# Performance work log

Hardware: AMD Instinct MI355X
Metric: run time of the kernel (lower is better)

The kernel has to match this reference:

```python
import jax, jax.numpy as jnp
import numpy as np

B, L, D_MODEL, H, H_DIM = 2, 4096, 768, 1, 128
D_K = H * H_DIM
F_LEN = L // 2 + 1
TEMP = 1.0
EPS = 1e-9
INV_SQRT_DK = float(1.0 / np.sqrt(H_DIM))


def _selector(xc, W1, b1, W2, b2, noise, temp):
    # xc: [B, h, d, F] complex. torch view_as_real(x.transpose(-1,-2))[..., 0] == real part.
    xr = jnp.real(jnp.swapaxes(xc, -1, -2))          # [B, h, F, d]
    h1 = jax.nn.relu(xr @ W1.T + b1)                 # [B, h, F, d//2]
    logit = h1 @ W2.T + b2                           # [B, h, F, 2]
    g = -jnp.log(-jnp.log(noise + EPS) + EPS)        # gumbel noise from uniform input
    z = jax.nn.softmax((logit + g) / temp, axis=-1)[..., 1]  # training mode: soft mask
    return z[..., None, :]                           # [B, h, 1, F]


def _forward(query, key, mask, Wq, bq, Wk, bk, qW1, qb1, qW2, qb2, kW1, kb1, kW2, kb2, q_noise, k_noise):
    nb, Lq = query.shape[0], query.shape[1]
    q = (query @ Wq.T + bq).reshape(nb, Lq, H, H_DIM).transpose(0, 2, 3, 1)  # [B, h, d, L]
    k = (key @ Wk.T + bk).reshape(nb, Lq, H, H_DIM).transpose(0, 2, 3, 1)
    q_tff = jnp.fft.rfft(q, axis=-1)                 # [B, h, d, F] complex
    k_tff = jnp.fft.rfft(k, axis=-1)
    q_m = _selector(q_tff, qW1, qb1, qW2, qb2, q_noise, TEMP)
    k_m = _selector(k_tff, kW1, kb1, kW2, kb2, k_noise, TEMP)
    qf = jnp.fft.irfft(q_tff * q_m, n=Lq, axis=-1)   # [B, h, d, L]
    kf = jnp.fft.irfft(k_tff * k_m, n=Lq, axis=-1)
    scores = jnp.einsum('bhdl,bhdm->bhlm', qf, kf) * INV_SQRT_DK  # [B, h, L, L]
    m = mask[:, None, :, :Lq]                        # [B, 1, 1, L]
    scores = jnp.where(m == 0, -1e9, scores)
    return jax.nn.softmax(scores, axis=-1)           # dropout omitted (eval/identity)


def setup_inputs() -> dict:
    key = jax.random.key(0)
    ks = jax.random.split(key, 12)
    s = 0.02
    return {
        'query': jax.random.normal(ks[0], (B, L, D_MODEL), jnp.float32),
        'key': jax.random.normal(ks[1], (B, L, D_MODEL), jnp.float32),
        'mask': jax.random.randint(ks[2], (B, 1, L), 0, 2, jnp.int32),
        'Wq': s * jax.random.normal(ks[3], (D_K, D_MODEL), jnp.float32),
        'bq': jnp.zeros((D_K,), jnp.float32),
        'Wk': s * jax.random.normal(ks[4], (D_K, D_MODEL), jnp.float32),
        'bk': jnp.zeros((D_K,), jnp.float32),
        'qW1': s * jax.random.normal(ks[5], (D_K // 2, D_K), jnp.float32),
        'qb1': jnp.zeros((D_K // 2,), jnp.float32),
        'qW2': s * jax.random.normal(ks[6], (2, D_K // 2), jnp.float32),
        'qb2': jnp.zeros((2,), jnp.float32),
        'kW1': s * jax.random.normal(ks[7], (D_K // 2, D_K), jnp.float32),
        'kb1': jnp.zeros((D_K // 2,), jnp.float32),
        'kW2': s * jax.random.normal(ks[8], (2, D_K // 2), jnp.float32),
        'kb2': jnp.zeros((2,), jnp.float32),
        'q_noise': jax.random.uniform(ks[9], (B, H, F_LEN, 2), jnp.float32),
        'k_noise': jax.random.uniform(ks[10], (B, H, F_LEN, 2), jnp.float32),
    }


def reference(query, key, mask, Wq, bq, Wk, bk, qW1, qb1, qW2, qb2, kW1, kb1, kW2, kb2, q_noise, k_noise):
    return _forward(query, key, mask, Wq, bq, Wk, bk, qW1, qb1, qW2, qb2, kW1, kb1, kW2, kb2, q_noise, k_noise)
```

## Files before the change

kernel.cpp:

```cpp
#include <hip/hip_runtime.h>
#include <hip/hip_bf16.h>

#define LL 4096
#define FL 2049
#define DKN 128
#define DMOD 768

#define TW_OFF   0
#define XT_OFF   4096
#define SPEC_OFF (4096 + 2097152)
#define Z_OFF    (SPEC_OFF + 2098176)
#define QKH_OFF  4207624
#define WH_OFF   (QKH_OFF + 6291456)

using bf16x8 = __attribute__((ext_vector_type(8))) short;
using f32x4  = __attribute__((ext_vector_type(4))) float;

__device__ __forceinline__ float2 cmul(float2 a, float2 b) {
    return make_float2(a.x * b.x - a.y * b.y, a.x * b.y + a.y * b.x);
}
__device__ __forceinline__ int SWZ(int a) { return a ^ ((a >> 4) & 15); }
__device__ __forceinline__ ushort f2bf(float f) {
    __hip_bfloat16 h = __float2bfloat16(f);
    return *(ushort*)&h;
}
__device__ __forceinline__ float bfbits(unsigned u) {
    union { unsigned i; float f; } x; x.i = u; return x.f;
}

__global__ void k_twiddle(float2* __restrict__ tw) {
    int j = blockIdx.x * 256 + threadIdx.x;
    if (j < 2048) {
        double a = -2.0 * 3.14159265358979323846 * (double)j / 4096.0;
        tw[j] = make_float2((float)cos(a), (float)sin(a));
    }
}

__global__ __launch_bounds__(256) void k_cvt(const float* __restrict__ s0,
                                             const float* __restrict__ s1,
                                             ushort* __restrict__ hi, int n) {
    const float* src = blockIdx.y ? s1 : s0;
    ushort* h = hi + (size_t)blockIdx.y * n;
    int i8 = (blockIdx.x * 256 + threadIdx.x) * 8;
    if (i8 >= n) return;
    float4 a = *(const float4*)&src[i8];
    float4 b = *(const float4*)&src[i8 + 4];
    float v[8] = {a.x, a.y, a.z, a.w, b.x, b.y, b.z, b.w};
    union { ushort us[8]; uint4 q; } ph;
#pragma unroll
    for (int u = 0; u < 8; u++) ph.us[u] = f2bf(v[u]);
    *(uint4*)&h[i8] = ph.q;
}

__global__ __launch_bounds__(256) void k_proj(const ushort* __restrict__ XH,
                                              const ushort* __restrict__ WH,
                                              const float* __restrict__ bq,
                                              const float* __restrict__ bk,
                                              float* __restrict__ xt) {
    int tz = blockIdx.z, b = blockIdx.y;
    int l0 = blockIdx.x * 64;
    int t = threadIdx.x, w = t >> 6, lane = t & 63;
    int g = lane >> 4, c = lane & 15;
    size_t xrow0 = ((size_t)(tz * 2 + b)) * LL + l0;
    const ushort* WHt = WH + (size_t)tz * DKN * DMOD;
    const float* bias = tz ? bk : bq;
    float* outp = xt + (size_t)(tz * 2 + b) * DKN * LL;
    f32x4 acc[2][4] = {};
    for (int ks = 0; ks < 24; ks++) {
        int kb = ks * 32 + g * 8;
        bf16x8 ah[2], xh[4];
#pragma unroll
        for (int dt = 0; dt < 2; dt++)
            ah[dt] = *(const bf16x8*)&WHt[(size_t)(w * 32 + dt * 16 + c) * DMOD + kb];
#pragma unroll
        for (int nt = 0; nt < 4; nt++)
            xh[nt] = *(const bf16x8*)&XH[(xrow0 + nt * 16 + c) * DMOD + kb];
#pragma unroll
        for (int dt = 0; dt < 2; dt++)
#pragma unroll
            for (int nt = 0; nt < 4; nt++)
                acc[dt][nt] = __builtin_amdgcn_mfma_f32_16x16x32_bf16(ah[dt], xh[nt], acc[dt][nt], 0, 0, 0);
    }
#pragma unroll
    for (int dt = 0; dt < 2; dt++)
#pragma unroll
        for (int r = 0; r < 4; r++) {
            int d = w * 32 + dt * 16 + g * 4 + r;
            float bd = bias[d];
#pragma unroll
            for (int nt = 0; nt < 4; nt++)
                outp[(size_t)d * LL + l0 + nt * 16 + c] = acc[dt][nt][r] + bd;
        }
}

template <int INV>
__global__ __launch_bounds__(512) void k_fft4(const float* __restrict__ xin,
                                              float2* __restrict__ spec,
                                              const float* __restrict__ zsel,
                                              float* __restrict__ xout,
                                              const float2* __restrict__ tw) {
    __shared__ float2 buf[4096];
    __shared__ float2 ltw[2048];
    int ser = blockIdx.x;
    int t   = threadIdx.x;
    for (int i = t; i < 2048; i += 512) ltw[i] = tw[i];
    if (!INV) {
        const float* x = xin + (size_t)ser * LL;
        for (int i = t; i < 4096; i += 512) buf[SWZ(i)] = make_float2(x[i], 0.f);
    } else {
        const float2* sp = spec + (size_t)ser * FL;
        const float*  zz = zsel + (size_t)(ser >> 7) * FL;
        for (int f = t; f < FL; f += 512) {
            float2 v = sp[f];
            float  m = zz[f];
            float2 vm = make_float2(v.x * m, v.y * m);
            buf[SWZ(f)] = vm;
            if (f > 0 && f < 2048) buf[SWZ(4096 - f)] = make_float2(vm.x, -vm.y);
        }
    }
    __syncthreads();
#pragma unroll
    for (int st = 0; st < 6; st++) {
        int Lm1 = (1 << (2 * st)) - 1;
        float2 x0[2], x1[2], x2[2], x3[2];
#pragma unroll
        for (int ii = 0; ii < 2; ii++) {
            int idx = t + 512 * ii;
            x0[ii] = buf[SWZ(idx)];
            x1[ii] = buf[SWZ(idx + 1024)];
            x2[ii] = buf[SWZ(idx + 2048)];
            x3[ii] = buf[SWZ(idx + 3072)];
        }
        __syncthreads();
#pragma unroll
        for (int ii = 0; ii < 2; ii++) {
            int idx = t + 512 * ii;
            int q = idx & Lm1;
            int r = idx - q;
            int wbase = q + (r << 2);
            int L = Lm1 + 1;
            float2 a0 = x0[ii], a1 = x1[ii], a2 = x2[ii], a3 = x3[ii];
            float2 t0 = make_float2(a0.x + a2.x, a0.y + a2.y);
            float2 t1 = make_float2(a0.x - a2.x, a0.y - a2.y);
            float2 t2 = make_float2(a1.x + a3.x, a1.y + a3.y);
            float2 t3 = make_float2(a1.x - a3.x, a1.y - a3.y);
            float2 y0 = make_float2(t0.x + t2.x, t0.y + t2.y);
            float2 y2 = make_float2(t0.x - t2.x, t0.y - t2.y);
            float2 y1, y3;
            if (!INV) {
                y1 = make_float2(t1.x + t3.y, t1.y - t3.x);
                y3 = make_float2(t1.x - t3.y, t1.y + t3.x);
            } else {
                y1 = make_float2(t1.x - t3.y, t1.y + t3.x);
                y3 = make_float2(t1.x + t3.y, t1.y - t3.x);
            }
            float2 w1 = ltw[r];
            float2 w2 = ltw[2 * r];
            if (INV) { w1.y = -w1.y; w2.y = -w2.y; }
            float2 w3 = cmul(w1, w2);
            buf[SWZ(wbase)]         = y0;
            buf[SWZ(wbase + L)]     = cmul(y1, w1);
            buf[SWZ(wbase + 2 * L)] = cmul(y2, w2);
            buf[SWZ(wbase + 3 * L)] = cmul(y3, w3);
        }
        __syncthreads();
    }
    if (!INV) {
        float2* sp = spec + (size_t)ser * FL;
        for (int f = t; f < FL; f += 512) sp[f] = buf[SWZ(f)];
    } else {
        float* xo = xout + (size_t)ser * LL;
        const float sc = 1.0f / 4096.0f;
        for (int i = t; i < 4096; i += 512) xo[i] = buf[SWZ(i)].x * sc;
    }
}

__global__ __launch_bounds__(256) void k_sel2(const float2* __restrict__ spec,
                                              const float* __restrict__ qW1,
                                              const float* __restrict__ qb1,
                                              const float* __restrict__ qW2,
                                              const float* __restrict__ qb2,
                                              const float* __restrict__ kW1,
                                              const float* __restrict__ kb1,
                                              const float* __restrict__ kW2,
                                              const float* __restrict__ kb2,
                                              const float* __restrict__ qnoise,
                                              const float* __restrict__ knoise,
                                              float* __restrict__ z) {
    int tz = blockIdx.z, b = blockIdx.y;
    int f0 = blockIdx.x * 64;
    const float* W1 = tz ? kW1 : qW1;
    const float* b1 = tz ? kb1 : qb1;
    const float* W2 = tz ? kW2 : qW2;
    const float* b2 = tz ? kb2 : qb2;
    const float* nz = tz ? knoise : qnoise;
    __shared__ float xr[64][132];
    const float2* sp = spec + (size_t)(tz * 2 + b) * DKN * FL;
    int t = threadIdx.x;
    {
        int d = t >> 1, half = t & 1;
        const float2* row = sp + (size_t)d * FL;
#pragma unroll
        for (int i2 = 0; i2 < 32; i2++) {
            int fi = f0 + half * 32 + i2;
            float v = (fi < FL) ? row[fi].x : 0.f;
            xr[half * 32 + i2][d] = v;
        }
    }
    __syncthreads();
    int lane = t & 63, fg = t >> 6;
    float acc[16];
    float bj = b1[lane];
#pragma unroll
    for (int ff = 0; ff < 16; ff++) acc[ff] = bj;
    const float4* w1r = (const float4*)&W1[(size_t)lane * 128];
    for (int d4 = 0; d4 < 32; d4++) {
        float4 wv = w1r[d4];
#pragma unroll
        for (int ff = 0; ff < 16; ff++) {
            float4 xv = *(const float4*)&xr[fg * 16 + ff][d4 * 4];
            acc[ff] = fmaf(xv.x, wv.x, acc[ff]);
            acc[ff] = fmaf(xv.y, wv.y, acc[ff]);
            acc[ff] = fmaf(xv.z, wv.z, acc[ff]);
            acc[ff] = fmaf(xv.w, wv.w, acc[ff]);
        }
    }
    float w2a = W2[lane], w2b = W2[64 + lane];
    float l0f = 0.f, l1f = 0.f;
#pragma unroll
    for (int ff = 0; ff < 16; ff++) {
        float h = fmaxf(acc[ff], 0.f);
        float l0 = h * w2a, l1 = h * w2b;
#pragma unroll
        for (int off = 32; off >= 1; off >>= 1) {
            l0 += __shfl_xor(l0, off);
            l1 += __shfl_xor(l1, off);
        }
        if (lane == ff) { l0f = l0; l1f = l1; }
    }
    if (lane < 16) {
        int f = f0 + fg * 16 + lane;
        if (f < FL) {
            float a0 = l0f + b2[0];
            float a1 = l1f + b2[1];
            const float* np = nz + ((size_t)b * FL + f) * 2;
            float g0 = -logf(-logf(np[0] + 1e-9f) + 1e-9f);
            float g1 = -logf(-logf(np[1] + 1e-9f) + 1e-9f);
            a0 += g0; a1 += g1;
            z[(size_t)(tz * 2 + b) * FL + f] = 1.f / (1.f + expf(a0 - a1));
        }
    }
}

__global__ __launch_bounds__(256) void k_tr(const float* __restrict__ xt,
                                            ushort* __restrict__ xtb) {
    __shared__ float s[64][129];
    int tb = blockIdx.y;
    int l0 = blockIdx.x * 64;
    int t  = threadIdx.x;
    const float* gp = xt + (size_t)tb * DKN * LL;
    int d = t >> 1, c0 = (t & 1) * 32;
#pragma unroll
    for (int j4 = 0; j4 < 8; j4++) {
        float4 v = *(const float4*)&gp[(size_t)d * LL + l0 + c0 + j4 * 4];
        s[c0 + j4 * 4 + 0][d] = v.x;
        s[c0 + j4 * 4 + 1][d] = v.y;
        s[c0 + j4 * 4 + 2][d] = v.z;
        s[c0 + j4 * 4 + 3][d] = v.w;
    }
    __syncthreads();
    int l = t >> 2, dc0 = (t & 3) * 32;
    ushort* o = xtb + (size_t)tb * LL * DKN + (size_t)(l0 + l) * DKN + dc0;
#pragma unroll
    for (int c8 = 0; c8 < 4; c8++) {
        union { ushort us[8]; uint4 v; } pk;
#pragma unroll
        for (int u = 0; u < 8; u++) pk.us[u] = f2bf(s[l][dc0 + c8 * 8 + u]);
        *(uint4*)&o[c8 * 8] = pk.v;
    }
}

#define SCOLS 4104
__global__ __launch_bounds__(512) void k_scores_soft(const ushort* __restrict__ xtb,
                                                     const int* __restrict__ mask,
                                                     float* __restrict__ out) {
    extern __shared__ char smem[];
    ushort* sbuf = (ushort*)smem;
    float*  wsum = (float*)(smem + 16 * SCOLS * 2);
    int b  = blockIdx.y;
    int l0 = blockIdx.x * 16;
    int t = threadIdx.x, w = t >> 6, lane = t & 63;
    int g = lane >> 4, c = lane & 15;
    const ushort* A = xtb + (size_t)b * LL * DKN;
    const ushort* B = xtb + (size_t)(2 + b) * LL * DKN;
    const int* mk = mask + (size_t)b * LL;
    const float sc = 0.08838834764831843f;
    bf16x8 af[4];
#pragma unroll
    for (int kk = 0; kk < 4; kk++)
        af[kk] = *(const bf16x8*)&A[(size_t)(l0 + c) * DKN + kk * 32 + g * 8];
    float rsum = 0.f;
    for (int mt = 0; mt < 8; mt++) {
        int m0 = w * 512 + mt * 64;
        f32x4 acc[4] = {};
#pragma unroll
        for (int kk = 0; kk < 4; kk++) {
            bf16x8 bfr[4];
#pragma unroll
            for (int nt = 0; nt < 4; nt++)
                bfr[nt] = *(const bf16x8*)&B[(size_t)(m0 + nt * 16 + c) * DKN + kk * 32 + g * 8];
#pragma unroll
            for (int nt = 0; nt < 4; nt++)
                acc[nt] = __builtin_amdgcn_mfma_f32_16x16x32_bf16(bfr[nt], af[kk], acc[nt], 0, 0, 0);
        }
#pragma unroll
        for (int nt = 0; nt < 4; nt++) {
            int mbase = m0 + nt * 16 + g * 4;
            int4 mv = *(const int4*)&mk[mbase];
            float e0 = mv.x ? __expf(acc[nt][0] * sc) : 0.f;
            float e1 = mv.y ? __expf(acc[nt][1] * sc) : 0.f;
            float e2 = mv.z ? __expf(acc[nt][2] * sc) : 0.f;
            float e3 = mv.w ? __expf(acc[nt][3] * sc) : 0.f;
            rsum += (e0 + e1) + (e2 + e3);
            uint2 pk;
            pk.x = (unsigned)f2bf(e0) | ((unsigned)f2bf(e1) << 16);
            pk.y = (unsigned)f2bf(e2) | ((unsigned)f2bf(e3) << 16);
            *(uint2*)&sbuf[(size_t)c * SCOLS + mbase] = pk;
        }
    }
    rsum += __shfl_xor(rsum, 16);
    rsum += __shfl_xor(rsum, 32);
    if (lane < 16) wsum[w * 16 + lane] = rsum;
    __syncthreads();
    float* ob = out + ((size_t)(b * LL + l0)) * LL;
    int col0 = w * 512 + lane * 8;
#pragma unroll 4
    for (int rr = 0; rr < 16; rr++) {
        float S = 0.f;
#pragma unroll
        for (int ww = 0; ww < 8; ww++) S += wsum[ww * 16 + rr];
        float* orow = ob + (size_t)rr * LL;
        uint4 v = *(const uint4*)&sbuf[(size_t)rr * SCOLS + col0];
        if (S > 0.f) {
            float inv = 1.0f / S;
            float4 r0, r1;
            r0.x = bfbits(v.x << 16) * inv;  r0.y = bfbits(v.x & 0xffff0000u) * inv;
            r0.z = bfbits(v.y << 16) * inv;  r0.w = bfbits(v.y & 0xffff0000u) * inv;
            r1.x = bfbits(v.z << 16) * inv;  r1.y = bfbits(v.z & 0xffff0000u) * inv;
            r1.z = bfbits(v.w << 16) * inv;  r1.w = bfbits(v.w & 0xffff0000u) * inv;
            *(float4*)&orow[col0] = r0;
            *(float4*)&orow[col0 + 4] = r1;
        } else {
            const float u = 2.44140625e-4f;
            float4 r = make_float4(u, u, u, u);
            *(float4*)&orow[col0] = r;
            *(float4*)&orow[col0 + 4] = r;
        }
    }
}

extern "C" void kernel_launch(void* const* d_in, const int* in_sizes, int n_in,
                              void* d_out, int out_size, void* d_ws, size_t ws_size,
                              hipStream_t stream) {
    (void)in_sizes; (void)n_in; (void)out_size; (void)ws_size;
    const float* query  = (const float*)d_in[0];
    const float* key    = (const float*)d_in[1];
    const int*   mask   = (const int*)d_in[2];
    const float* Wq     = (const float*)d_in[3];
    const float* bq     = (const float*)d_in[4];
    const float* Wk     = (const float*)d_in[5];
    const float* bk     = (const float*)d_in[6];
    const float* qW1    = (const float*)d_in[7];
    const float* qb1    = (const float*)d_in[8];
    const float* qW2    = (const float*)d_in[9];
    const float* qb2    = (const float*)d_in[10];
    const float* kW1    = (const float*)d_in[11];
    const float* kb1    = (const float*)d_in[12];
    const float* kW2    = (const float*)d_in[13];
    const float* kb2    = (const float*)d_in[14];
    const float* qnoise = (const float*)d_in[15];
    const float* knoise = (const float*)d_in[16];

    float*  ws   = (float*)d_ws;
    float2* tw   = (float2*)(ws + TW_OFF);
    float*  xt   = ws + XT_OFF;
    float2* spec = (float2*)(ws + SPEC_OFF);
    ushort* xtb  = (ushort*)(ws + SPEC_OFF);
    float*  zsel = ws + Z_OFF;
    ushort* qkh  = (ushort*)(ws + QKH_OFF);
    ushort* wh   = (ushort*)(ws + WH_OFF);
    float*  out  = (float*)d_out;

    const int NQK = 2 * LL * DMOD;
    const int NW  = DKN * DMOD;

    k_twiddle<<<dim3(8), dim3(256), 0, stream>>>(tw);
    k_cvt<<<dim3(NQK / 2048, 2), dim3(256), 0, stream>>>(query, key, qkh, NQK);
    k_cvt<<<dim3(NW / 2048, 2), dim3(256), 0, stream>>>(Wq, Wk, wh, NW);
    k_proj<<<dim3(64, 2, 2), dim3(256), 0, stream>>>(qkh, wh, bq, bk, xt);
    k_fft4<0><<<dim3(512), dim3(512), 0, stream>>>(xt, spec, nullptr, nullptr, tw);
    k_sel2<<<dim3(33, 2, 2), dim3(256), 0, stream>>>(spec, qW1, qb1, qW2, qb2,
                                                     kW1, kb1, kW2, kb2, qnoise, knoise, zsel);
    k_fft4<1><<<dim3(512), dim3(512), 0, stream>>>(nullptr, spec, zsel, xt, tw);
    k_tr<<<dim3(64, 4), dim3(256), 0, stream>>>(xt, xtb);
    size_t smem = 16 * SCOLS * 2 + 8 * 16 * 4;
    k_scores_soft<<<dim3(256, 2), dim3(512), smem, stream>>>(xtb, mask, out);
}
```

Measured before the change: 357.5 us.

## Keep softmax exponentials in registers and double scores block width

The scores kernel now uses 1024 threads (16 waves), and each wave covers 256 columns instead of 512. The exponentials stay in registers instead of being staged as bf16 in a ~131KB shared buffer, so that LDS round trip and its limit on occupancy go away, and the bf16 rounding of probabilities is dropped. Output is now written straight from the MFMA layout as float4 stores per lane. Those stores are less contiguous per row than the old staged, coalesced writes, and holding 64 floats per thread raises register pressure.

Measured after the change: 347.7 us. 2.7% less time.

```diff
diff --git a/kernel.cpp b/kernel.cpp
--- a/kernel.cpp
+++ b/kernel.cpp
@@ -23,9 +23,6 @@
 __device__ __forceinline__ ushort f2bf(float f) {
     __hip_bfloat16 h = __float2bfloat16(f);
     return *(ushort*)&h;
-}
-__device__ __forceinline__ float bfbits(unsigned u) {
-    union { unsigned i; float f; } x; x.i = u; return x.f;
 }
 
 __global__ void k_twiddle(float2* __restrict__ tw) {
@@ -280,13 +277,10 @@
     }
 }
 
-#define SCOLS 4104
-__global__ __launch_bounds__(512) void k_scores_soft(const ushort* __restrict__ xtb,
-                                                     const int* __restrict__ mask,
-                                                     float* __restrict__ out) {
-    extern __shared__ char smem[];
-    ushort* sbuf = (ushort*)smem;
-    float*  wsum = (float*)(smem + 16 * SCOLS * 2);
+__global__ __launch_bounds__(1024, 4) void k_scores_soft(const ushort* __restrict__ xtb,
+                                                         const int* __restrict__ mask,
+                                                         float* __restrict__ out) {
+    __shared__ float wsum[16][16];
     int b  = blockIdx.y;
     int l0 = blockIdx.x * 16;
     int t = threadIdx.x, w = t >> 6, lane = t & 63;
@@ -299,9 +293,11 @@
 #pragma unroll
     for (int kk = 0; kk < 4; kk++)
         af[kk] = *(const bf16x8*)&A[(size_t)(l0 + c) * DKN + kk * 32 + g * 8];
+    float ev[4][4][4];
     float rsum = 0.f;
-    for (int mt = 0; mt < 8; mt++) {
-        int m0 = w * 512 + mt * 64;
+#pragma unroll
+    for (int mt = 0; mt < 4; mt++) {
+        int m0 = w * 256 + mt * 64;
         f32x4 acc[4] = {};
 #pragma unroll
         for (int kk = 0; kk < 4; kk++) {
@@ -321,42 +317,34 @@
             float e1 = mv.y ? __expf(acc[nt][1] * sc) : 0.f;
             float e2 = mv.z ? __expf(acc[nt][2] * sc) : 0.f;
             float e3 = mv.w ? __expf(acc[nt][3] * sc) : 0.f;
+            ev[mt][nt][0] = e0; ev[mt][nt][1] = e1;
+            ev[mt][nt][2] = e2; ev[mt][nt][3] = e3;
             rsum += (e0 + e1) + (e2 + e3);
-            uint2 pk;
-            pk.x = (unsigned)f2bf(e0) | ((unsigned)f2bf(e1) << 16);
-            pk.y = (unsigned)f2bf(e2) | ((unsigned)f2bf(e3) << 16);
-            *(uint2*)&sbuf[(size_t)c * SCOLS + mbase] = pk;
         }
     }
     rsum += __shfl_xor(rsum, 16);
     rsum += __shfl_xor(rsum, 32);
-    if (lane < 16) wsum[w * 16 + lane] = rsum;
+    if (lane < 16) wsum[w][lane] = rsum;
     __syncthreads();
-    float* ob = out + ((size_t)(b * LL + l0)) * LL;
-    int col0 = w * 512 + lane * 8;
-#pragma unroll 4
-    for (int rr = 0; rr < 16; rr++) {
-        float S = 0.f;
-#pragma unroll
-        for (int ww = 0; ww < 8; ww++) S += wsum[ww * 16 + rr];
-        float* orow = ob + (size_t)rr * LL;
-        uint4 v = *(const uint4*)&sbuf[(size_t)rr * SCOLS + col0];
-        if (S > 0.f) {
-            float inv = 1.0f / S;
-            float4 r0, r1;
-            r0.x = bfbits(v.x << 16) * inv;  r0.y = bfbits(v.x & 0xffff0000u) * inv;
-            r0.z = bfbits(v.y << 16) * inv;  r0.w = bfbits(v.y & 0xffff0000u) * inv;
-            r1.x = bfbits(v.z << 16) * inv;  r1.y = bfbits(v.z & 0xffff0000u) * inv;
-            r1.z = bfbits(v.w << 16) * inv;  r1.w = bfbits(v.w & 0xffff0000u) * inv;
-            *(float4*)&orow[col0] = r0;
-            *(float4*)&orow[col0 + 4] = r1;
-        } else {
-            const float u = 2.44140625e-4f;
-            float4 r = make_float4(u, u, u, u);
-            *(float4*)&orow[col0] = r;
-            *(float4*)&orow[col0 + 4] = r;
-        }
-    }
+    float S = 0.f;
+#pragma unroll
+    for (int ww = 0; ww < 16; ww++) S += wsum[ww][c];
+    bool ok = (S > 0.f);
+    float inv = ok ? 1.0f / S : 0.f;
+    const float u = 2.44140625e-4f;
+    float* orow = out + ((size_t)(b * LL + l0 + c)) * LL;
+#pragma unroll
+    for (int mt = 0; mt < 4; mt++)
+#pragma unroll
+        for (int nt = 0; nt < 4; nt++) {
+            int mbase = w * 256 + mt * 64 + nt * 16 + g * 4;
+            float4 r;
+            r.x = ok ? ev[mt][nt][0] * inv : u;
+            r.y = ok ? ev[mt][nt][1] * inv : u;
+            r.z = ok ? ev[mt][nt][2] * inv : u;
+            r.w = ok ? ev[mt][nt][3] * inv : u;
+            *(float4*)&orow[mbase] = r;
+        }
 }
 
 extern "C" void kernel_launch(void* const* d_in, const int* in_sizes, int n_in,
@@ -403,6 +391,5 @@
                                                      kW1, kb1, kW2, kb2, qnoise, knoise, zsel);
     k_fft4<1><<<dim3(512), dim3(512), 0, stream>>>(nullptr, spec, zsel, xt, tw);
     k_tr<<<dim3(64, 4), dim3(256), 0, stream>>>(xt, xtb);
-    size_t smem = 16 * SCOLS * 2 + 8 * 16 * 4;
-    k_scores_soft<<<dim3(256, 2), dim3(512), smem, stream>>>(xtb, mask, out);
-}
+    k_scores_soft<<<dim3(256, 2), dim3(1024), 0, stream>>>(xtb, mask, out);
+}
```
